# Kernel optimization log

Measured on AMD Instinct MI355X. Metric: run time of the kernel, lower is better.

## Reference

```python
import jax, jax.numpy as jnp
import numpy as np

BS, BT, DIM = 32, 1024, 512
NEG_MASK = -1000000.0  # masked_fill value for b/i scores
NEG_SPAN = -1000.0     # lower-triangle fill for span matrix


def setup_inputs() -> dict:
    key = jax.random.key(0)
    ks = jax.random.split(key, 6)
    s = 1.0 / np.sqrt(DIM)  # xavier-ish scale
    return {
        "x": jax.random.normal(ks[0], (BS, DIM), jnp.float32),
        "sen_vecs": jax.random.normal(ks[1], (BS, BT, DIM), jnp.float32),
        "sen_mask": jnp.ones((BS, BT), jnp.int32),
        "Wb": jax.random.normal(ks[2], (DIM, DIM), jnp.float32) * s,
        "bb": jnp.zeros((DIM,), jnp.float32),
        "Wi": jax.random.normal(ks[3], (DIM, DIM), jnp.float32) * s,
        "bi": jnp.zeros((DIM,), jnp.float32),
        "Wo": jax.random.normal(ks[4], (DIM, DIM), jnp.float32) * s,
        "bo": jnp.zeros((DIM,), jnp.float32),
    }


def reference(x, sen_vecs, sen_mask, Wb, bb, Wi, bi, Wo, bo):
    def proj_scores(W, b):
        # torch Linear: sen_vecs @ W.T + b, then dot with x -> [bs, bt]
        h = jnp.einsum('btd,ed->bte', sen_vecs, W) + b
        return jnp.einsum('bte,be->bt', h, x)

    m0 = (sen_mask == 0)
    sb = jnp.where(m0, NEG_MASK, proj_scores(Wb, bb))  # [bs,bt]
    si = jnp.where(m0, NEG_MASK, proj_scores(Wi, bi))
    so = jnp.where(m0, 0.0, proj_scores(Wo, bo))

    # per-step logsumexp over the 3 BIO labels; the CRF-style recursions
    # f[t] = lse(f[t-1] + bio[t-1]) collapse to cumsums since f[t-1] is scalar.
    lse = jax.nn.logsumexp(jnp.stack([sb, si, so], axis=-1), axis=-1)  # [bs,bt]
    z = jnp.zeros((sb.shape[0], 1), sb.dtype)
    fwd = jnp.concatenate([z, jnp.cumsum(lse, axis=1)], axis=1)                      # [bs,bt+1]
    bwd = jnp.concatenate([jnp.flip(jnp.cumsum(jnp.flip(lse, 1), 1), 1), z], axis=1)  # [bs,bt+1]
    full = fwd[:, -1:]

    # prefix sums of scores_i: Ci[t] = sum(si[:t]); sum(si[s:e]) = Ci[e]-Ci[s]
    Ci = jnp.concatenate([z, jnp.cumsum(si, axis=1)], axis=1)  # [bs,bt+1]

    A = sb + fwd[:, :-1] - Ci[:, :-1] - full   # indexed by span start s
    B = Ci[:, :-1] + bwd[:, 1:] + so           # indexed by span end e
    span = A[:, :, None] + B[:, None, :]       # [bs, bt, bt], rows=s, cols=e
    tri = jnp.triu(jnp.ones((sb.shape[1], sb.shape[1]), bool))  # e >= s
    return jnp.where(tri[None], span, jnp.asarray(NEG_SPAN, span.dtype))
```

## Files before the change

### kernel.cpp

```cpp
#include <hip/hip_runtime.h>
#include <math.h>


#define BS 32
#define BT 1024
#define DIM 512
#define ECH 4
#define EC  (DIM / ECH)
#define NEG_MASK -1000000.0f
#define NEG_SPAN -1000.0f

typedef float f4 __attribute__((ext_vector_type(4)));

__global__ __launch_bounds__(256) void k1_proj(
    const float* __restrict__ x,
    const float* __restrict__ Wb, const float* __restrict__ bb,
    const float* __restrict__ Wi, const float* __restrict__ bi,
    const float* __restrict__ Wo, const float* __restrict__ bo,
    float* __restrict__ Yp, float* __restrict__ C)
{
    const int w = blockIdx.y;
    const int z = blockIdx.z;
    const float* __restrict__ W    = (w == 0) ? Wb : (w == 1) ? Wi : Wo;
    const float* __restrict__ bias = (w == 0) ? bb : (w == 1) ? bi : bo;
    const int tid = threadIdx.x;

    if (blockIdx.x == 8) {
        if (z != 0) return;
        const int v = tid >> 6, l = tid & 63;
        for (int b = v; b < BS; b += 4) {
            float acc = 0.f;
            for (int e = l; e < DIM; e += 64) acc += bias[e] * x[b * DIM + e];
            #pragma unroll
            for (int o = 32; o >= 1; o >>= 1) acc += __shfl_xor(acc, o);
            if (l == 0) C[w * BS + b] = acc;
        }
        return;
    }

    __shared__ float xs[BS * EC];
    const int e0 = z * EC;
    for (int k = tid; k < BS * EC; k += 256) {
        const int b = k >> 7, e = k & (EC - 1);
        xs[k] = x[b * DIM + e0 + e];
    }
    __syncthreads();

    const int d0 = blockIdx.x * 64;
    const int dt = tid & 63, bg = tid >> 6;
    const int d  = d0 + dt;

    float acc[8];
    #pragma unroll
    for (int i = 0; i < 8; i++) acc[i] = 0.f;
    for (int e = 0; e < EC; e++) {
        const float wv = W[(e0 + e) * DIM + d];
        #pragma unroll
        for (int i = 0; i < 8; i++)
            acc[i] += wv * xs[(bg * 8 + i) * EC + e];
    }
    #pragma unroll
    for (int i = 0; i < 8; i++)
        Yp[((z * 3 + w) * BS + bg * 8 + i) * DIM + d] = acc[i];
}

__global__ __launch_bounds__(256) void k2a_scores(
    const float* __restrict__ sv, const int* __restrict__ mask,
    const float* __restrict__ Yp, const float* __restrict__ C,
    float* __restrict__ SB, float* __restrict__ SI, float* __restrict__ SO,
    float* __restrict__ LSE)
{
    __shared__ float ys[3 * DIM];
    const int blk = blockIdx.x;
    const int b   = blk >> 7;
    const int t0  = (blk & 127) * 8;
    const int tid = threadIdx.x;

    for (int k = tid; k < 3 * DIM; k += 256) {
        const int w = k >> 9, d = k & (DIM - 1);
        float s = 0.f;
        #pragma unroll
        for (int zz = 0; zz < ECH; zz++)
            s += Yp[((zz * 3 + w) * BS + b) * DIM + d];
        ys[k] = s;
    }
    __syncthreads();

    const int v = tid >> 6, l = tid & 63;

    const f4* __restrict__ yb4 = (const f4*)(ys);
    const f4* __restrict__ yi4 = (const f4*)(ys + DIM);
    const f4* __restrict__ yo4 = (const f4*)(ys + 2 * DIM);

    const f4 yb1 = yb4[l], yb2 = yb4[64 + l];
    const f4 yi1 = yi4[l], yi2 = yi4[64 + l];
    const f4 yo1 = yo4[l], yo2 = yo4[64 + l];

    const int tA = t0 + v, tB = t0 + v + 4;
    const f4* __restrict__ svA = (const f4*)(sv + (size_t)(b * BT + tA) * DIM);
    const f4* __restrict__ svB = (const f4*)(sv + (size_t)(b * BT + tB) * DIM);

    const f4 a1 = __builtin_nontemporal_load(svA + l);
    const f4 a2 = __builtin_nontemporal_load(svA + 64 + l);
    const f4 b1 = __builtin_nontemporal_load(svB + l);
    const f4 b2 = __builtin_nontemporal_load(svB + 64 + l);

    #define DOT(p, q, y1, y2) \
        (p.x*y1.x + p.y*y1.y + p.z*y1.z + p.w*y1.w + \
         q.x*y2.x + q.y*y2.y + q.z*y2.z + q.w*y2.w)

    float rAB = DOT(a1, a2, yb1, yb2);
    float rAI = DOT(a1, a2, yi1, yi2);
    float rAO = DOT(a1, a2, yo1, yo2);
    float rBB = DOT(b1, b2, yb1, yb2);
    float rBI = DOT(b1, b2, yi1, yi2);
    float rBO = DOT(b1, b2, yo1, yo2);
    #undef DOT

    #pragma unroll
    for (int o = 32; o >= 1; o >>= 1) {
        rAB += __shfl_xor(rAB, o);
        rAI += __shfl_xor(rAI, o);
        rAO += __shfl_xor(rAO, o);
        rBB += __shfl_xor(rBB, o);
        rBI += __shfl_xor(rBI, o);
        rBO += __shfl_xor(rBO, o);
    }

    if (l == 0) {
        const float cb = C[0 * BS + b];
        const float ci = C[1 * BS + b];
        const float co = C[2 * BS + b];
        #pragma unroll
        for (int r = 0; r < 2; r++) {
            const int t = r ? tB : tA;
            float sb = (r ? rBB : rAB) + cb;
            float si = (r ? rBI : rAI) + ci;
            float so = (r ? rBO : rAO) + co;
            if (mask[b * BT + t] == 0) { sb = NEG_MASK; si = NEG_MASK; so = 0.f; }
            const float m   = fmaxf(sb, fmaxf(si, so));
            const float lse = m + logf(expf(sb - m) + expf(si - m) + expf(so - m));
            const int idx = b * BT + t;
            SB[idx] = sb; SI[idx] = si; SO[idx] = so; LSE[idx] = lse;
        }
    }
}

__global__ __launch_bounds__(1024) void k2b_scan(
    const float* __restrict__ SB, const float* __restrict__ SI,
    const float* __restrict__ SO, const float* __restrict__ LSE,
    float* __restrict__ A, float* __restrict__ Bv)
{
    __shared__ float sL[BT], sS[BT];
    const int b = blockIdx.x, t = threadIdx.x;
    const float l0 = LSE[b * BT + t];
    const float s0 = SI[b * BT + t];
    sL[t] = l0; sS[t] = s0;
    __syncthreads();

    for (int off = 1; off < BT; off <<= 1) {
        float a = 0.f, c = 0.f;
        if (t >= off) { a = sL[t - off]; c = sS[t - off]; }
        __syncthreads();
        if (t >= off) { sL[t] += a; sS[t] += c; }
        __syncthreads();
    }

    const float total = sL[BT - 1];
    const float pl = sL[t] - l0;
    const float ps = sS[t] - s0;
    A [b * BT + t] = SB[b * BT + t] + pl - ps - total;
    Bv[b * BT + t] = ps + (total - sL[t]) + SO[b * BT + t];
}

__global__ __launch_bounds__(256) void k3_span(
    const float* __restrict__ A, const float* __restrict__ Bv,
    f4* __restrict__ out)
{
    const int idx = blockIdx.x * 256 + threadIdx.x;
    const int b  = idx >> 18;
    const int r  = idx & 0x3FFFF;
    const int i  = r >> 8;
    const int j4 = r & 255;

    const float a = A[b * BT + i];
    const f4 bb4 = ((const f4*)(Bv + b * BT))[j4];
    const int j = j4 * 4;
    f4 o;
    o.x = (j     >= i) ? a + bb4.x : NEG_SPAN;
    o.y = (j + 1 >= i) ? a + bb4.y : NEG_SPAN;
    o.z = (j + 2 >= i) ? a + bb4.z : NEG_SPAN;
    o.w = (j + 3 >= i) ? a + bb4.w : NEG_SPAN;
    __builtin_nontemporal_store(o, out + idx);
}

extern "C" void kernel_launch(void* const* d_in, const int* in_sizes, int n_in,
                              void* d_out, int out_size, void* d_ws, size_t ws_size,
                              hipStream_t stream) {
    const float* x   = (const float*)d_in[0];
    const float* sv  = (const float*)d_in[1];
    const int*   msk = (const int*)  d_in[2];
    const float* Wb  = (const float*)d_in[3];
    const float* bb  = (const float*)d_in[4];
    const float* Wi  = (const float*)d_in[5];
    const float* bi  = (const float*)d_in[6];
    const float* Wo  = (const float*)d_in[7];
    const float* bo  = (const float*)d_in[8];

    float* ws = (float*)d_ws;
    float* Yp  = ws;
    float* C   = ws + ECH * 3 * BS * DIM;
    float* SB  = C + 512;
    float* SI  = SB + BS * BT;
    float* SO  = SI + BS * BT;
    float* LSE = SO + BS * BT;
    float* A   = LSE + BS * BT;
    float* Bv  = A + BS * BT;

    k1_proj   <<<dim3(9, 3, ECH), 256, 0, stream>>>(x, Wb, bb, Wi, bi, Wo, bo, Yp, C);
    k2a_scores<<<BS * 128, 256, 0, stream>>>(sv, msk, Yp, C, SB, SI, SO, LSE);
    k2b_scan  <<<BS, 1024, 0, stream>>>(SB, SI, SO, LSE, A, Bv);
    k3_span   <<<32768, 256, 0, stream>>>(A, Bv, (f4*)d_out);
}
```

Baseline: 268.8 us.

## Batch more rows per block in scores, warp-shuffle scan, row-per-wave span writer

The scores kernel now has each wave handle four timesteps instead of two, halving the block count and reducing how often the per-batch projection vector is rebuilt in shared memory. The scan kernel replaces the barrier-heavy shared-memory Hillis-Steele scan with a wave-level shuffle scan plus a 16-entry cross-wave combine. The span kernel assigns one output row per wave, so each lane writes four vectors per row and the A value is loaded once per row. Together these aim to cut redundant setup and synchronisation, at the cost of more registers per thread and fewer blocks in flight for the memory-bound kernels.

Result: no change. 265.2 us (-1.3%).

```diff
diff --git a/kernel.cpp b/kernel.cpp
--- a/kernel.cpp
+++ b/kernel.cpp
@@ -72,8 +72,8 @@
 {
     __shared__ float ys[3 * DIM];
     const int blk = blockIdx.x;
-    const int b   = blk >> 7;
-    const int t0  = (blk & 127) * 8;
+    const int b   = blk >> 6;
+    const int t0  = (blk & 63) * 16;
     const int tid = threadIdx.x;
 
     for (int k = tid; k < 3 * DIM; k += 256) {
@@ -96,35 +96,36 @@
     const f4 yi1 = yi4[l], yi2 = yi4[64 + l];
     const f4 yo1 = yo4[l], yo2 = yo4[64 + l];
 
-    const int tA = t0 + v, tB = t0 + v + 4;
-    const f4* __restrict__ svA = (const f4*)(sv + (size_t)(b * BT + tA) * DIM);
-    const f4* __restrict__ svB = (const f4*)(sv + (size_t)(b * BT + tB) * DIM);
-
-    const f4 a1 = __builtin_nontemporal_load(svA + l);
-    const f4 a2 = __builtin_nontemporal_load(svA + 64 + l);
-    const f4 b1 = __builtin_nontemporal_load(svB + l);
-    const f4 b2 = __builtin_nontemporal_load(svB + 64 + l);
+    f4 s1[4], s2[4];
+    #pragma unroll
+    for (int r = 0; r < 4; r++) {
+        const f4* __restrict__ p =
+            (const f4*)(sv + (size_t)(b * BT + t0 + v + 4 * r) * DIM);
+        s1[r] = __builtin_nontemporal_load(p + l);
+        s2[r] = __builtin_nontemporal_load(p + 64 + l);
+    }
 
     #define DOT(p, q, y1, y2) \
         (p.x*y1.x + p.y*y1.y + p.z*y1.z + p.w*y1.w + \
          q.x*y2.x + q.y*y2.y + q.z*y2.z + q.w*y2.w)
 
-    float rAB = DOT(a1, a2, yb1, yb2);
-    float rAI = DOT(a1, a2, yi1, yi2);
-    float rAO = DOT(a1, a2, yo1, yo2);
-    float rBB = DOT(b1, b2, yb1, yb2);
-    float rBI = DOT(b1, b2, yi1, yi2);
-    float rBO = DOT(b1, b2, yo1, yo2);
+    float rB[4], rI[4], rO[4];
+    #pragma unroll
+    for (int r = 0; r < 4; r++) {
+        rB[r] = DOT(s1[r], s2[r], yb1, yb2);
+        rI[r] = DOT(s1[r], s2[r], yi1, yi2);
+        rO[r] = DOT(s1[r], s2[r], yo1, yo2);
+    }
     #undef DOT
 
     #pragma unroll
     for (int o = 32; o >= 1; o >>= 1) {
-        rAB += __shfl_xor(rAB, o);
-        rAI += __shfl_xor(rAI, o);
-        rAO += __shfl_xor(rAO, o);
-        rBB += __shfl_xor(rBB, o);
-        rBI += __shfl_xor(rBI, o);
-        rBO += __shfl_xor(rBO, o);
+        #pragma unroll
+        for (int r = 0; r < 4; r++) {
+            rB[r] += __shfl_xor(rB[r], o);
+            rI[r] += __shfl_xor(rI[r], o);
+            rO[r] += __shfl_xor(rO[r], o);
+        }
     }
 
     if (l == 0) {
@@ -132,11 +133,11 @@
         const float ci = C[1 * BS + b];
         const float co = C[2 * BS + b];
         #pragma unroll
-        for (int r = 0; r < 2; r++) {
-            const int t = r ? tB : tA;
-            float sb = (r ? rBB : rAB) + cb;
-            float si = (r ? rBI : rAI) + ci;
-            float so = (r ? rBO : rAO) + co;
+        for (int r = 0; r < 4; r++) {
+            const int t = t0 + v + 4 * r;
+            float sb = rB[r] + cb;
+            float si = rI[r] + ci;
+            float so = rO[r] + co;
             if (mask[b * BT + t] == 0) { sb = NEG_MASK; si = NEG_MASK; so = 0.f; }
             const float m   = fmaxf(sb, fmaxf(si, so));
             const float lse = m + logf(expf(sb - m) + expf(si - m) + expf(so - m));
@@ -151,47 +152,63 @@
     const float* __restrict__ SO, const float* __restrict__ LSE,
     float* __restrict__ A, float* __restrict__ Bv)
 {
-    __shared__ float sL[BT], sS[BT];
+    __shared__ float wL[16], wS[16];
     const int b = blockIdx.x, t = threadIdx.x;
+    const int wv = t >> 6, l = t & 63;
+
     const float l0 = LSE[b * BT + t];
     const float s0 = SI[b * BT + t];
-    sL[t] = l0; sS[t] = s0;
+
+    float cl = l0, cs = s0;
+    #pragma unroll
+    for (int off = 1; off < 64; off <<= 1) {
+        const float al = __shfl_up(cl, off);
+        const float as = __shfl_up(cs, off);
+        if (l >= off) { cl += al; cs += as; }
+    }
+    if (l == 63) { wL[wv] = cl; wS[wv] = cs; }
     __syncthreads();
 
-    for (int off = 1; off < BT; off <<= 1) {
-        float a = 0.f, c = 0.f;
-        if (t >= off) { a = sL[t - off]; c = sS[t - off]; }
-        __syncthreads();
-        if (t >= off) { sL[t] += a; sS[t] += c; }
-        __syncthreads();
-    }
-
-    const float total = sL[BT - 1];
-    const float pl = sL[t] - l0;
-    const float ps = sS[t] - s0;
-    A [b * BT + t] = SB[b * BT + t] + pl - ps - total;
-    Bv[b * BT + t] = ps + (total - sL[t]) + SO[b * BT + t];
+    float basL = 0.f, basS = 0.f, totL = 0.f, totS = 0.f;
+    #pragma unroll
+    for (int w = 0; w < 16; w++) {
+        const float a = wL[w], c = wS[w];
+        totL += a; totS += c;
+        if (w < wv) { basL += a; basS += c; }
+    }
+
+    const float incL = cl + basL;
+    const float incS = cs + basS;
+    const float pl = incL - l0;
+    const float ps = incS - s0;
+    A [b * BT + t] = SB[b * BT + t] + pl - ps - totL;
+    Bv[b * BT + t] = ps + (totL - incL) + SO[b * BT + t];
 }
 
 __global__ __launch_bounds__(256) void k3_span(
     const float* __restrict__ A, const float* __restrict__ Bv,
     f4* __restrict__ out)
 {
-    const int idx = blockIdx.x * 256 + threadIdx.x;
-    const int b  = idx >> 18;
-    const int r  = idx & 0x3FFFF;
-    const int i  = r >> 8;
-    const int j4 = r & 255;
-
-    const float a = A[b * BT + i];
-    const f4 bb4 = ((const f4*)(Bv + b * BT))[j4];
-    const int j = j4 * 4;
-    f4 o;
-    o.x = (j     >= i) ? a + bb4.x : NEG_SPAN;
-    o.y = (j + 1 >= i) ? a + bb4.y : NEG_SPAN;
-    o.z = (j + 2 >= i) ? a + bb4.z : NEG_SPAN;
-    o.w = (j + 3 >= i) ? a + bb4.w : NEG_SPAN;
-    __builtin_nontemporal_store(o, out + idx);
+    const int g = blockIdx.x * 4 + (threadIdx.x >> 6);
+    const int l = threadIdx.x & 63;
+    const int i = g & 1023;
+
+    const float a = A[g];
+    const f4* __restrict__ bv = (const f4*)(Bv + (g & ~1023));
+    f4* __restrict__ orow = out + ((size_t)g << 8);
+
+    #pragma unroll
+    for (int k = 0; k < 4; k++) {
+        const int j4 = l + 64 * k;
+        const f4 b4 = bv[j4];
+        const int j = j4 * 4;
+        f4 o;
+        o.x = (j     >= i) ? a + b4.x : NEG_SPAN;
+        o.y = (j + 1 >= i) ? a + b4.y : NEG_SPAN;
+        o.z = (j + 2 >= i) ? a + b4.z : NEG_SPAN;
+        o.w = (j + 3 >= i) ? a + b4.w : NEG_SPAN;
+        __builtin_nontemporal_store(o, orow + j4);
+    }
 }
 
 extern "C" void kernel_launch(void* const* d_in, const int* in_sizes, int n_in,
@@ -218,7 +235,7 @@
     float* Bv  = A + BS * BT;
 
     k1_proj   <<<dim3(9, 3, ECH), 256, 0, stream>>>(x, Wb, bb, Wi, bi, Wo, bo, Yp, C);
-    k2a_scores<<<BS * 128, 256, 0, stream>>>(sv, msk, Yp, C, SB, SI, SO, LSE);
+    k2a_scores<<<BS * 64, 256, 0, stream>>>(sv, msk, Yp, C, SB, SI, SO, LSE);
     k2b_scan  <<<BS, 1024, 0, stream>>>(SB, SI, SO, LSE, A, Bv);
-    k3_span   <<<32768, 256, 0, stream>>>(A, Bv, (f4*)d_out);
-}
+    k3_span   <<<8192, 256, 0, stream>>>(A, Bv, (f4*)d_out);
+}
```
